# Optimization experiments

Measured on AMD Instinct MI355X. Metric: run time of the kernel, lower is better.

## Reference

```python
import jax, jax.numpy as jnp
import numpy as np
import math

H, KV, D = 16, 8, 256
SOFT_CAP = 50.0
WINDOW = 1024
EMBED = 3584


def _rope_tables(seq_len):
    inv_freq = 1.0 / (10000.0 ** (jnp.arange(0, D, 2, dtype=jnp.float32) / D))
    pos = jnp.arange(seq_len, dtype=jnp.float32)
    freqs = jnp.outer(pos, inv_freq)            # [S, D/2]
    emb = jnp.concatenate([freqs, freqs], -1)   # [S, D]
    return jnp.cos(emb), jnp.sin(emb)


def _apply_rope(x, cos, sin):
    # x: [B, S, h, D]; cos/sin: [S, D]
    x1, x2 = jnp.split(x, 2, axis=-1)
    rot = jnp.concatenate([-x2, x1], axis=-1)
    c = cos[None, :, None, :]
    s = sin[None, :, None, :]
    return x * c + rot * s


def setup_inputs() -> dict:
    key = jax.random.key(0)
    ks = jax.random.split(key, 5)
    B, S = 2, 2048
    std = 0.02
    return {
        "hidden_states": jax.random.normal(ks[0], (B, S, EMBED), jnp.float32),
        "Wq": jax.random.normal(ks[1], (EMBED, H * D), jnp.float32) * std,
        "Wk": jax.random.normal(ks[2], (EMBED, KV * D), jnp.float32) * std,
        "Wv": jax.random.normal(ks[3], (EMBED, KV * D), jnp.float32) * std,
        "Wo": jax.random.normal(ks[4], (H * D, EMBED), jnp.float32) * std,
    }


def reference(hidden_states, Wq, Wk, Wv, Wo):
    B, S, _ = hidden_states.shape
    scale = 1.0 / math.sqrt(D)

    q = (hidden_states @ Wq).reshape(B, S, H, D)
    k = (hidden_states @ Wk).reshape(B, S, KV, D)
    v = (hidden_states @ Wv).reshape(B, S, KV, D)

    cos, sin = _rope_tables(S)
    q = _apply_rope(q, cos, sin)
    k = _apply_rope(k, cos, sin)

    # GQA: repeat kv heads to match query heads
    rep = H // KV
    k = jnp.repeat(k, rep, axis=2)  # [B, S, H, D]
    v = jnp.repeat(v, rep, axis=2)

    attn = jnp.einsum('bqhd,bkhd->bhqk', q, k) * scale
    # logit soft-cap
    attn = jnp.tanh(attn / SOFT_CAP) * SOFT_CAP
    # symmetric sliding-window mask |i-j| <= WINDOW (as in source)
    pos = jnp.arange(S)
    mask = jnp.abs(pos[:, None] - pos[None, :]) <= WINDOW  # [S, S]
    attn = jnp.where(mask[None, None, :, :], attn, -jnp.inf)

    probs = jax.nn.softmax(attn, axis=-1)
    out = jnp.einsum('bhqk,bkhd->bqhd', probs, v).reshape(B, S, H * D)
    return out @ Wo
```

## Files before the change

kernel.cpp:

```cpp
#include <hip/hip_runtime.h>
#include <stdint.h>

typedef unsigned short U16;
typedef float f32x4 __attribute__((ext_vector_type(4)));
typedef __bf16 bf16x8 __attribute__((ext_vector_type(8)));

static __device__ __forceinline__ U16 f2bf(float x) {
  union { float f; unsigned u; } v; v.f = x;
  unsigned r = v.u + 0x7FFFu + ((v.u >> 16) & 1u);
  return (U16)(r >> 16);
}
static __device__ __forceinline__ float bf2f(U16 h) {
  union { unsigned u; float f; } v; v.u = ((unsigned)h) << 16;
  return v.f;
}

static __device__ __forceinline__ void gload_lds16(const void* g, void* l) {
  __builtin_amdgcn_global_load_lds(
      (const __attribute__((address_space(1))) void*)g,
      (__attribute__((address_space(3))) void*)l, 16, 0, 0);
}

#define SBAR() __builtin_amdgcn_sched_barrier(0)

__global__ __launch_bounds__(256) void k_convert(const float* __restrict__ src,
                                                 U16* __restrict__ dst, long n) {
  long base = ((long)blockIdx.x * 256 + threadIdx.x) * 8;
  if (base >= n) return;
  const float4* s = (const float4*)(src + base);
  float4 a = s[0], b = s[1];
  U16 o[8] = { f2bf(a.x), f2bf(a.y), f2bf(a.z), f2bf(a.w),
               f2bf(b.x), f2bf(b.y), f2bf(b.z), f2bf(b.w) };
  *(uint4*)(dst + base) = *(const uint4*)o;
}

__global__ __launch_bounds__(256) void k_transpose(const float* __restrict__ src,
                                                   U16* __restrict__ dst,
                                                   int K, int N) {
  __shared__ U16 tile[32][33];
  int n0 = blockIdx.x * 32, k0 = blockIdx.y * 32;
  int tx = threadIdx.x & 31, ty = threadIdx.x >> 5;
#pragma unroll
  for (int r = 0; r < 4; ++r) {
    int k = k0 + ty + r * 8;
    tile[ty + r * 8][tx] = f2bf(src[(long)k * N + n0 + tx]);
  }
  __syncthreads();
#pragma unroll
  for (int r = 0; r < 4; ++r) {
    int n = n0 + ty + r * 8;
    dst[(long)n * K + k0 + tx] = tile[tx][ty + r * 8];
  }
}

__global__ __launch_bounds__(256) void k_vtrans(const U16* __restrict__ QKV,
                                                U16* __restrict__ VT) {
  __shared__ U16 tile[32][33];
  int s0 = blockIdx.x * 32, d0 = blockIdx.y * 32, bk = blockIdx.z;
  int b = bk >> 3, kvh = bk & 7;
  int tx = threadIdx.x & 31, ty = threadIdx.x >> 5;
  const U16* src = QKV + (long)(b * 2048) * 8192 + 6144 + kvh * 256;
#pragma unroll
  for (int r = 0; r < 4; ++r) {
    int s = s0 + ty + r * 8;
    tile[ty + r * 8][tx] = src[(long)s * 8192 + d0 + tx];
  }
  __syncthreads();
  long tbase = ((long)bk * 64 + (s0 >> 5)) * 8192;
#pragma unroll
  for (int r = 0; r < 4; ++r) {
    int d = d0 + ty + r * 8;
    VT[tbase + d * 32 + tx] = tile[tx][ty + r * 8];
  }
}

__global__ __launch_bounds__(256) void k_rope_tables(float* __restrict__ cosT,
                                                     float* __restrict__ sinT) {
  int i = blockIdx.x * 256 + threadIdx.x;
  int s = i >> 7, d = i & 127;
  float freq = expf(-9.210340371976184f * (float)d / 128.0f);
  float ang = (float)s * freq;
  cosT[i] = cosf(ang);
  sinT[i] = sinf(ang);
}

__global__ __launch_bounds__(256) void k_rope(U16* __restrict__ qkv,
                                              const float* __restrict__ cosT,
                                              const float* __restrict__ sinT) {
  int i = blockIdx.x * 256 + threadIdx.x;
  int d = i & 127;
  int hh = (i >> 7) % 24;
  int row = i / 3072;
  int s = row & 2047;
  int col = (hh < 16) ? hh * 256 + d : 4096 + (hh - 16) * 256 + d;
  long base = (long)row * 8192 + col;
  float c = cosT[s * 128 + d], sn = sinT[s * 128 + d];
  float x1 = bf2f(qkv[base]), x2 = bf2f(qkv[base + 128]);
  qkv[base]       = f2bf(x1 * c - x2 * sn);
  qkv[base + 128] = f2bf(x2 * c + x1 * sn);
}

template <int F32OUT>
__global__ __launch_bounds__(512, 1) void k_gemm8(const U16* __restrict__ A,
                                                  const U16* __restrict__ Bt,
                                                  void* __restrict__ Cv,
                                                  int M, int N, int K) {
  __shared__ __align__(16) U16 Asl[2][2][128 * 64];
  __shared__ __align__(16) U16 Bsl[2][2][128 * 64];
  int nwg = gridDim.x * gridDim.y;
  int flat = blockIdx.y * gridDim.x + blockIdx.x;
  int cpx = nwg >> 3;
  int swz = (flat & 7) * cpx + (flat >> 3);
  int bx = swz % gridDim.x, by = swz / gridDim.x;
  int t = threadIdx.x, lane = t & 63, w = t >> 6;
  int m0 = by * 256, n0 = bx * 256;
  int wm = w >> 2, wn = w & 3;
  int l15 = lane & 15, l4 = lane >> 4;
  int lofs = (l15 * 4 + l4) * 16;

  f32x4 acc[8][4] = {};
  int T = K >> 6;

  int sr = lane >> 2, sc4 = (lane & 3) * 8;
  int fA0 = (w >> 1) * 16 + sr, kA0 = (w & 1) * 32 + sc4;
  int fA1 = ((8 + w) >> 1) * 16 + sr, kA1 = ((8 + w) & 1) * 32 + sc4;
  const U16* aj0 = A + (long)(m0 + fA0) * K + kA0;
  const U16* aj1 = A + (long)(m0 + fA1) * K + kA1;
  const U16* bj0 = Bt + (long)(n0 + fA0) * K + kA0;
  const U16* bj1 = Bt + (long)(n0 + fA1) * K + kA1;

  auto stageH = [&](int op, int kt, int h) {
    int buf = kt & 1;
    int ktc = (kt < T) ? kt : 0;
    long off = (long)ktc * 64 + (long)h * 128 * K;
    if (op == 0) {
      gload_lds16(aj0 + off, (char*)&Asl[buf][h][0] + w * 1024);
      gload_lds16(aj1 + off, (char*)&Asl[buf][h][0] + 8192 + w * 1024);
    } else {
      gload_lds16(bj0 + off, (char*)&Bsl[buf][h][0] + w * 1024);
      gload_lds16(bj1 + off, (char*)&Bsl[buf][h][0] + 8192 + w * 1024);
    }
  };

  bf16x8 Ar[4][2], Bq[2][2][2];

  auto readA = [&](int buf, int r) {
    const char* base = (const char*)&Asl[buf][wm][0] + lofs;
#pragma unroll
    for (int i = 0; i < 4; ++i)
#pragma unroll
      for (int kk = 0; kk < 2; ++kk)
        Ar[i][kk] = *(const bf16x8*)(base + ((r * 4 + i) * 2 + kk) * 1024);
  };
  auto readB = [&](int buf, int c) {
    const char* base = (const char*)&Bsl[buf][wn >> 1][0] + lofs;
#pragma unroll
    for (int j = 0; j < 2; ++j)
#pragma unroll
      for (int kk = 0; kk < 2; ++kk)
        Bq[c][j][kk] = *(const bf16x8*)(base + (((wn & 1) * 4 + c * 2 + j) * 2 + kk) * 1024);
  };
  auto mfmaQ = [&](int r, int c) {
    __builtin_amdgcn_s_setprio(1);
#pragma unroll
    for (int i = 0; i < 4; ++i)
#pragma unroll
      for (int j = 0; j < 2; ++j) {
        int m = r * 4 + i, n = c * 2 + j;
        acc[m][n] = __builtin_amdgcn_mfma_f32_16x16x32_bf16(Ar[i][0], Bq[c][j][0], acc[m][n], 0, 0, 0);
        acc[m][n] = __builtin_amdgcn_mfma_f32_16x16x32_bf16(Ar[i][1], Bq[c][j][1], acc[m][n], 0, 0, 0);
      }
    __builtin_amdgcn_s_setprio(0);
  };

#define PH_SYNC() do { SBAR(); __builtin_amdgcn_s_barrier(); \
    asm volatile("s_waitcnt lgkmcnt(0)" ::: "memory"); SBAR(); } while (0)
#define PH_END() do { SBAR(); __builtin_amdgcn_s_barrier(); SBAR(); } while (0)

  stageH(0, 0, 0); stageH(0, 0, 1); stageH(1, 0, 0); stageH(1, 0, 1);
  stageH(1, 1, 0); stageH(0, 1, 0);
  asm volatile("s_waitcnt vmcnt(4)" ::: "memory");
  SBAR(); __builtin_amdgcn_s_barrier(); SBAR();

  for (int base = 0; base < T; base += 2) {
    readA(0, 0); readB(0, 0);
    stageH(0, base + 1, 1);
    PH_SYNC(); mfmaQ(0, 0); PH_END();
    readB(0, 1);
    stageH(1, base + 1, 1);
    PH_SYNC(); mfmaQ(0, 1); PH_END();
    readA(0, 1);
    stageH(1, base + 2, 0);
    PH_SYNC(); mfmaQ(1, 1); PH_END();
    stageH(0, base + 2, 0);
    PH_SYNC(); mfmaQ(1, 0);
    asm volatile("s_waitcnt vmcnt(4)" ::: "memory");
    PH_END();
    readA(1, 0); readB(1, 0);
    stageH(0, base + 2, 1);
    PH_SYNC(); mfmaQ(0, 0); PH_END();
    readB(1, 1);
    stageH(1, base + 2, 1);
    PH_SYNC(); mfmaQ(0, 1); PH_END();
    readA(1, 1);
    stageH(1, base + 3, 0);
    PH_SYNC(); mfmaQ(1, 1); PH_END();
    stageH(0, base + 3, 0);
    PH_SYNC(); mfmaQ(1, 0);
    asm volatile("s_waitcnt vmcnt(4)" ::: "memory");
    PH_END();
  }

#undef PH_SYNC
#undef PH_END

#pragma unroll
  for (int m = 0; m < 8; ++m)
#pragma unroll
    for (int jj = 0; jj < 4; ++jj) {
      int row = m0 + wm * 128 + m * 16 + l4 * 4 + jj;
      if (F32OUT) {
        float* cp = (float*)Cv + (long)row * N + n0 + wn * 64 + l15;
#pragma unroll
        for (int n = 0; n < 4; ++n) cp[n * 16] = acc[m][n][jj];
      } else {
        U16* cp = (U16*)Cv + (long)row * N + n0 + wn * 64 + l15;
#pragma unroll
        for (int n = 0; n < 4; ++n) cp[n * 16] = f2bf(acc[m][n][jj]);
      }
    }
}

__global__ __launch_bounds__(256) void k_attn(const U16* __restrict__ QKV,
                                              const U16* __restrict__ VT,
                                              U16* __restrict__ O) {
  __shared__ __align__(16) U16 Ks[2][32 * 256];
  __shared__ __align__(16) U16 Vs[2][256 * 32];
  __shared__ __align__(16) U16 Plds[4][16 * 40];
  int t = threadIdx.x, lane = t & 63, w = t >> 6;
  int flat = blockIdx.x + 32 * (blockIdx.y + 16 * blockIdx.z);
  int l = (flat & 7) * 128 + (flat >> 3);
  int qb = l & 31, h = (l >> 5) & 15, b = l >> 9;
  int s0 = qb * 64;
  int kvh = h >> 1;
  long rowOff = (long)b * 2048 * 8192;
  const U16* Qb = QKV + rowOff + h * 256;
  const U16* Kb = QKV + rowOff + 4096 + kvh * 256;
  const U16* VTb = VT + (long)(b * 8 + kvh) * 64 * 8192;

  int l15 = lane & 15, l4 = lane >> 4;
  int lofs = (l15 * 4 + l4) * 16;

  bf16x8 qf[8];
  {
    const U16* qp = Qb + (long)(s0 + w * 16 + l15) * 8192 + l4 * 8;
#pragma unroll
    for (int kc = 0; kc < 8; ++kc) qf[kc] = *(const bf16x8*)(qp + kc * 32);
  }
  asm volatile("s_waitcnt vmcnt(0)" ::: "memory");

  f32x4 acc[16] = {};
  float mrun = -1e30f, lrun = 0.0f;
  int qpos = s0 + w * 16 + l15;
  int qlo = s0 + w * 16, qhi = qlo + 15;

  int kstart = s0 - 1024; if (kstart < 0) kstart = 0;
  int kend = s0 + 64 + 1024; if (kend > 2048) kend = 2048;

  int sl15 = (t >> 2) & 15, sl4 = t & 3;
  int offK[4], offV[4];
#pragma unroll
  for (int i = 0; i < 4; ++i) {
    int f = i * 4 + w;
    offK[i] = ((f >> 3) * 16 + sl15) * 8192 + (f & 7) * 32 + sl4 * 8;
    offV[i] = (f * 16 + sl15) * 32 + sl4 * 8;
  }

  const U16* kb = Kb + (long)kstart * 8192;
  const U16* vt0 = VTb + (long)(kstart >> 5) * 8192;

  auto stage = [&](int buf) {
#pragma unroll
    for (int i = 0; i < 4; ++i)
      gload_lds16(kb + offK[i], (char*)&Ks[buf][0] + i * 4096 + w * 1024);
#pragma unroll
    for (int i = 0; i < 4; ++i)
      gload_lds16(vt0 + offV[i], (char*)&Vs[buf][0] + i * 4096 + w * 1024);
    kb += (long)32 * 8192;
    vt0 += 8192;
  };

  auto compute = [&](int buf, int k0) {
    f32x4 sAcc[2] = {};
    const char* Kc = (const char*)&Ks[buf][0] + lofs;
    __builtin_amdgcn_s_setprio(1);
#pragma unroll
    for (int kc = 0; kc < 8; ++kc) {
      bf16x8 a0 = *(const bf16x8*)(Kc + kc * 1024);
      bf16x8 a1 = *(const bf16x8*)(Kc + (8 + kc) * 1024);
      sAcc[0] = __builtin_amdgcn_mfma_f32_16x16x32_bf16(a0, qf[kc], sAcc[0], 0, 0, 0);
      sAcc[1] = __builtin_amdgcn_mfma_f32_16x16x32_bf16(a1, qf[kc], sAcc[1], 0, 0, 0);
    }
    __builtin_amdgcn_s_setprio(0);
    float sv[8];
#pragma unroll
    for (int mp = 0; mp < 2; ++mp)
#pragma unroll
      for (int jj = 0; jj < 4; ++jj) {
        float ex = __expf(sAcc[mp][jj] * 0.0025f);
        sv[mp * 4 + jj] = fmaf(-100.0f, __builtin_amdgcn_rcpf(ex + 1.0f), 50.0f);
      }
    bool full = ((qhi - k0) <= 1024) && ((k0 + 31 - qlo) <= 1024);
    if (!full) {
#pragma unroll
      for (int mp = 0; mp < 2; ++mp)
#pragma unroll
        for (int jj = 0; jj < 4; ++jj) {
          int key = k0 + mp * 16 + l4 * 4 + jj;
          int dd = qpos - key;
          if (dd < -1024 || dd > 1024) sv[mp * 4 + jj] = -3e38f;
        }
    }
    float tmax = sv[0];
#pragma unroll
    for (int i = 1; i < 8; ++i) tmax = fmaxf(tmax, sv[i]);
    tmax = fmaxf(tmax, __shfl_xor(tmax, 16));
    tmax = fmaxf(tmax, __shfl_xor(tmax, 32));
    bool skipall = __all((tmax <= mrun + 8.0f) ? 1 : 0) != 0;
    float mnew = skipall ? mrun : fmaxf(mrun, tmax);
    float pex[8];
    float psum = 0.0f;
#pragma unroll
    for (int i = 0; i < 8; ++i) { pex[i] = __expf(sv[i] - mnew); psum += pex[i]; }
    psum += __shfl_xor(psum, 16);
    psum += __shfl_xor(psum, 32);
    if (skipall) {
      lrun += psum;
    } else {
      float esc = __expf(mrun - mnew);
      f32x4 ev;
#pragma unroll
      for (int jj = 0; jj < 4; ++jj) ev[jj] = __shfl(esc, l4 * 4 + jj);
#pragma unroll
      for (int n = 0; n < 16; ++n) acc[n] *= ev;
      lrun = lrun * esc + psum;
      mrun = mnew;
    }
#pragma unroll
    for (int mp = 0; mp < 2; ++mp)
#pragma unroll
      for (int j2 = 0; j2 < 2; ++j2) {
        unsigned lo = f2bf(pex[mp * 4 + j2 * 2]);
        unsigned hi = f2bf(pex[mp * 4 + j2 * 2 + 1]);
        *(unsigned*)&Plds[w][l15 * 40 + mp * 16 + l4 * 4 + j2 * 2] = lo | (hi << 16);
      }
    asm volatile("s_waitcnt lgkmcnt(0)" ::: "memory");
    __builtin_amdgcn_sched_barrier(0);
    bf16x8 pa = *(const bf16x8*)&Plds[w][l15 * 40 + l4 * 8];
    const char* Vc = (const char*)&Vs[buf][0] + lofs;
    __builtin_amdgcn_s_setprio(1);
#pragma unroll
    for (int n = 0; n < 16; ++n) {
      bf16x8 vb = *(const bf16x8*)(Vc + n * 1024);
      acc[n] = __builtin_amdgcn_mfma_f32_16x16x32_bf16(pa, vb, acc[n], 0, 0, 0);
    }
    __builtin_amdgcn_s_setprio(0);
  };

  int cur = 0;
  stage(0);
  for (int k0 = kstart; k0 < kend - 32; k0 += 32) {
    stage(cur ^ 1);
    asm volatile("s_waitcnt vmcnt(8)" ::: "memory");
    __builtin_amdgcn_s_barrier();
    __builtin_amdgcn_sched_barrier(0);
    compute(cur, k0);
    __builtin_amdgcn_s_barrier();
    cur ^= 1;
  }
  asm volatile("s_waitcnt vmcnt(0)" ::: "memory");
  __builtin_amdgcn_s_barrier();
  __builtin_amdgcn_sched_barrier(0);
  compute(cur, kend - 32);

  f32x4 linv;
#pragma unroll
  for (int jj = 0; jj < 4; ++jj) linv[jj] = 1.0f / __shfl(lrun, l4 * 4 + jj);
#pragma unroll
  for (int jj = 0; jj < 4; ++jj) {
    int row = s0 + w * 16 + l4 * 4 + jj;
    U16* op = O + ((long)b * 2048 + row) * 4096 + h * 256 + l15;
#pragma unroll
    for (int n = 0; n < 16; ++n) op[n * 16] = f2bf(acc[n][jj] * linv[jj]);
  }
}

extern "C" void kernel_launch(void* const* d_in, const int* in_sizes, int n_in,
                              void* d_out, int out_size, void* d_ws, size_t ws_size,
                              hipStream_t stream) {
  if (n_in < 5) return;
  const float* hid = (const float*)d_in[0];
  const float* Wq  = (const float*)d_in[1];
  const float* Wk  = (const float*)d_in[2];
  const float* Wv  = (const float*)d_in[3];
  const float* Wo  = (const float*)d_in[4];

  char* ws = (char*)d_ws;
  size_t off = 0;
  auto alloc = [&](size_t bytes) {
    char* p = ws + off;
    off += (bytes + 255) & ~(size_t)255;
    return p;
  };
  float* cosT = (float*)alloc((size_t)2048 * 128 * 4);
  float* sinT = (float*)alloc((size_t)2048 * 128 * 4);
  U16*   Xb   = (U16*)alloc((size_t)4096 * 3584 * 2);
  U16*   Wt   = (U16*)alloc((size_t)8192 * 3584 * 2);
  U16*   QKV  = (U16*)alloc((size_t)4096 * 8192 * 2);
  if (off > ws_size) return;
  U16* VT   = Xb;
  U16* Wot  = Xb;
  U16* AttO = Wt;

  k_convert<<<7168, 256, 0, stream>>>(hid, Xb, (long)4096 * 3584);
  k_transpose<<<dim3(128, 112), 256, 0, stream>>>(Wq, Wt, 3584, 4096);
  k_transpose<<<dim3(64, 112), 256, 0, stream>>>(Wk, Wt + (size_t)4096 * 3584, 3584, 2048);
  k_transpose<<<dim3(64, 112), 256, 0, stream>>>(Wv, Wt + (size_t)6144 * 3584, 3584, 2048);
  k_rope_tables<<<1024, 256, 0, stream>>>(cosT, sinT);
  k_gemm8<0><<<dim3(32, 16), 512, 0, stream>>>(Xb, Wt, QKV, 4096, 8192, 3584);
  k_vtrans<<<dim3(64, 8, 16), 256, 0, stream>>>(QKV, VT);
  k_rope<<<49152, 256, 0, stream>>>(QKV, cosT, sinT);
  k_attn<<<dim3(32, 16, 2), 256, 0, stream>>>(QKV, VT, AttO);
  k_transpose<<<dim3(112, 128), 256, 0, stream>>>(Wo, Wot, 4096, 3584);
  k_gemm8<1><<<dim3(14, 16), 512, 0, stream>>>(AttO, Wot, d_out, 4096, 3584, 4096);
}
```

Baseline: 688.8 us.

## Fuse RoPE into QKV GEMM epilogue by remapping wave column ownership

Removes the standalone RoPE kernel and applies the rotation inside the QKV GEMM epilogue for Q and K columns. To make that work, each wave's B-fragment mapping is changed so it holds column d and d+128 of the same 256-wide head, letting it rotate pairs in registers before writing bf16. This saves a full read-modify-write pass over the Q/K part of the QKV buffer and one kernel launch. The cost is extra cos/sin table loads in the epilogue and a changed store pattern, where each wave now writes two 32-column strips 128 apart.

```diff
diff --git a/kernel.cpp b/kernel.cpp
--- a/kernel.cpp
+++ b/kernel.cpp
@@ -84,26 +84,12 @@
   sinT[i] = sinf(ang);
 }
 
-__global__ __launch_bounds__(256) void k_rope(U16* __restrict__ qkv,
-                                              const float* __restrict__ cosT,
-                                              const float* __restrict__ sinT) {
-  int i = blockIdx.x * 256 + threadIdx.x;
-  int d = i & 127;
-  int hh = (i >> 7) % 24;
-  int row = i / 3072;
-  int s = row & 2047;
-  int col = (hh < 16) ? hh * 256 + d : 4096 + (hh - 16) * 256 + d;
-  long base = (long)row * 8192 + col;
-  float c = cosT[s * 128 + d], sn = sinT[s * 128 + d];
-  float x1 = bf2f(qkv[base]), x2 = bf2f(qkv[base + 128]);
-  qkv[base]       = f2bf(x1 * c - x2 * sn);
-  qkv[base + 128] = f2bf(x2 * c + x1 * sn);
-}
-
-template <int F32OUT>
+template <int EPI>
 __global__ __launch_bounds__(512, 1) void k_gemm8(const U16* __restrict__ A,
                                                   const U16* __restrict__ Bt,
                                                   void* __restrict__ Cv,
+                                                  const float* __restrict__ cosT,
+                                                  const float* __restrict__ sinT,
                                                   int M, int N, int K) {
   __shared__ __align__(16) U16 Asl[2][2][128 * 64];
   __shared__ __align__(16) U16 Bsl[2][2][128 * 64];
@@ -153,12 +139,12 @@
         Ar[i][kk] = *(const bf16x8*)(base + ((r * 4 + i) * 2 + kk) * 1024);
   };
   auto readB = [&](int buf, int c) {
-    const char* base = (const char*)&Bsl[buf][wn >> 1][0] + lofs;
+    const char* base = (const char*)&Bsl[buf][c][0] + lofs;
 #pragma unroll
     for (int j = 0; j < 2; ++j)
 #pragma unroll
       for (int kk = 0; kk < 2; ++kk)
-        Bq[c][j][kk] = *(const bf16x8*)(base + (((wn & 1) * 4 + c * 2 + j) * 2 + kk) * 1024);
+        Bq[c][j][kk] = *(const bf16x8*)(base + ((2 * wn + j) * 2 + kk) * 1024);
   };
   auto mfmaQ = [&](int r, int c) {
     __builtin_amdgcn_s_setprio(1);
@@ -214,19 +200,35 @@
 #undef PH_SYNC
 #undef PH_END
 
+  bool doRope = (EPI == 0) && (n0 < 6144);
 #pragma unroll
   for (int m = 0; m < 8; ++m)
 #pragma unroll
     for (int jj = 0; jj < 4; ++jj) {
       int row = m0 + wm * 128 + m * 16 + l4 * 4 + jj;
-      if (F32OUT) {
-        float* cp = (float*)Cv + (long)row * N + n0 + wn * 64 + l15;
-#pragma unroll
-        for (int n = 0; n < 4; ++n) cp[n * 16] = acc[m][n][jj];
-      } else {
-        U16* cp = (U16*)Cv + (long)row * N + n0 + wn * 64 + l15;
-#pragma unroll
-        for (int n = 0; n < 4; ++n) cp[n * 16] = f2bf(acc[m][n][jj]);
+      int s2 = row & 2047;
+#pragma unroll
+      for (int j = 0; j < 2; ++j) {
+        float lo = acc[m][j][jj];
+        float hi = acc[m][2 + j][jj];
+        int cl = wn * 32 + j * 16 + l15;
+        if (EPI == 0) {
+          if (doRope) {
+            int d = cl;
+            float co = cosT[s2 * 128 + d];
+            float si = sinT[s2 * 128 + d];
+            float o0 = lo * co - hi * si;
+            float o1 = hi * co + lo * si;
+            lo = o0; hi = o1;
+          }
+          U16* cp = (U16*)Cv + (long)row * N + n0 + cl;
+          cp[0] = f2bf(lo);
+          cp[128] = f2bf(hi);
+        } else {
+          float* cp = (float*)Cv + (long)row * N + n0 + cl;
+          cp[0] = lo;
+          cp[128] = hi;
+        }
       }
     }
 }
@@ -427,10 +429,9 @@
   k_transpose<<<dim3(64, 112), 256, 0, stream>>>(Wk, Wt + (size_t)4096 * 3584, 3584, 2048);
   k_transpose<<<dim3(64, 112), 256, 0, stream>>>(Wv, Wt + (size_t)6144 * 3584, 3584, 2048);
   k_rope_tables<<<1024, 256, 0, stream>>>(cosT, sinT);
-  k_gemm8<0><<<dim3(32, 16), 512, 0, stream>>>(Xb, Wt, QKV, 4096, 8192, 3584);
+  k_gemm8<0><<<dim3(32, 16), 512, 0, stream>>>(Xb, Wt, QKV, cosT, sinT, 4096, 8192, 3584);
   k_vtrans<<<dim3(64, 8, 16), 256, 0, stream>>>(QKV, VT);
-  k_rope<<<49152, 256, 0, stream>>>(QKV, cosT, sinT);
   k_attn<<<dim3(32, 16, 2), 256, 0, stream>>>(QKV, VT, AttO);
   k_transpose<<<dim3(112, 128), 256, 0, stream>>>(Wo, Wot, 4096, 3584);
-  k_gemm8<1><<<dim3(14, 16), 512, 0, stream>>>(AttO, Wot, d_out, 4096, 3584, 4096);
-}
+  k_gemm8<1><<<dim3(14, 16), 512, 0, stream>>>(AttO, Wot, d_out, cosT, sinT, 4096, 3584, 4096);
+}
```

Result: no change. 676.9 us (-1.7%).
